# Kernel tuning notes

Hardware: AMD Instinct MI355X
Metric: run time of the kernel (lower is better)

## Reference

```python
import jax, jax.numpy as jnp
import numpy as np

E, D_IN, D_OUT, N = 8, 1024, 1024, 8192

def setup_inputs() -> dict:
    key = jax.random.key(0)
    ks = jax.random.split(key, 5)
    s_in = 1.0 / np.sqrt(D_IN)
    x = jax.random.normal(ks[0], (N, D_IN), dtype=jnp.float32)
    We = jax.random.uniform(ks[1], (E, D_IN, D_OUT), dtype=jnp.float32, minval=-s_in, maxval=s_in)
    be = jax.random.uniform(ks[2], (E, D_OUT), dtype=jnp.float32, minval=-s_in, maxval=s_in)
    Wg = jax.random.uniform(ks[3], (D_IN, E), dtype=jnp.float32, minval=-s_in, maxval=s_in)
    bg = jax.random.uniform(ks[4], (E,), dtype=jnp.float32, minval=-s_in, maxval=s_in)
    return {"x": x, "We": We, "be": be, "Wg": Wg, "bg": bg}

def reference(x, We, be, Wg, bg):
    # experts_outputs: [N, E, D_OUT] (stacked per-expert Linear outputs)
    expert_out = jnp.einsum('ni,eio->neo', x, We) + be[None, :, :]
    # gate: softmax over experts, [N, E]
    gate = jax.nn.softmax(x @ Wg + bg, axis=1)
    # weighted combine (bmm of [N,1,E] x [N,E,D_OUT]) -> [N, D_OUT]
    return jnp.einsum('ne,neo->no', gate, expert_out)
```

## Files before the change

kernel.cpp:

```cpp
#include <hip/hip_runtime.h>
#include <hip/hip_bf16.h>
#include <cstdint>

#define NTOK 8192
#define DIN  1024
#define DOUT 1024
#define NEXP 8

typedef __attribute__((ext_vector_type(8)))  __bf16 bf16x8;
typedef __attribute__((ext_vector_type(4)))  float  f32x4;

__device__ __forceinline__ unsigned short f2bf(float f) {
    unsigned int u = __builtin_bit_cast(unsigned int, f);
    u += 0x7FFFu + ((u >> 16) & 1u);
    return (unsigned short)(u >> 16);
}

__device__ __forceinline__ void cp16(const void* gsrc, void* ldst) {
    __builtin_amdgcn_global_load_lds(
        (const __attribute__((address_space(1))) void*)gsrc,
        (__attribute__((address_space(3))) void*)ldst,
        16, 0, 0);
}

#define BAR() asm volatile("s_barrier" ::: "memory")

__global__ __launch_bounds__(256) void prep_kernel(
    const float* __restrict__ x, const float* __restrict__ We,
    const float* __restrict__ Wg, const float* __restrict__ bg,
    unsigned short* __restrict__ xb, unsigned short* __restrict__ wt,
    float* __restrict__ g)
{
    __shared__ float smem[12416];

    int t = threadIdx.x;

    if (blockIdx.x < 2048) {
        unsigned short* tile = (unsigned short*)smem;
        int b = blockIdx.x;
        int e  = b >> 8;
        int kt = (b >> 4) & 15;
        int ot = b & 15;

        const float* src = We + ((size_t)e << 20) + (size_t)(kt * 64) * DOUT + ot * 64;
        unsigned short* dst = wt + ((size_t)e << 20) + (size_t)(ot * 64) * DIN + kt * 64;

        int kl = t >> 2;
        int og = (t & 3) * 16;
#pragma unroll
        for (int c = 0; c < 4; ++c) {
            int o = og + c * 4;
            float4 v = *(const float4*)&src[(size_t)kl * DOUT + o];
            ushort4 u;
            u.x = f2bf(v.x); u.y = f2bf(v.y); u.z = f2bf(v.z); u.w = f2bf(v.w);
            *(ushort4*)&tile[kl * 72 + o] = u;
        }
        __syncthreads();
        int ol = t >> 2;
        int kg = (t & 3) * 16;
        unsigned short tmp[16];
#pragma unroll
        for (int i = 0; i < 16; ++i) tmp[i] = tile[(kg + i) * 72 + ol];
        *(uint4*)&dst[(size_t)ol * DIN + kg]     = *(uint4*)&tmp[0];
        *(uint4*)&dst[(size_t)ol * DIN + kg + 8] = *(uint4*)&tmp[8];
    } else {
        float* WgL = smem;
        float* xL  = smem + 8192;
        int n0 = (blockIdx.x - 2048) * 32;

#pragma unroll
        for (int q = 0; q < 8; ++q) {
            int fidx = q * 256 + t;
            int k  = fidx >> 1;
            int eh = (fidx & 1) * 4;
            float4 v = *(const float4*)&Wg[(size_t)k * 8 + eh];
            WgL[(eh + 0) * 1024 + k] = v.x;
            WgL[(eh + 1) * 1024 + k] = v.y;
            WgL[(eh + 2) * 1024 + k] = v.z;
            WgL[(eh + 3) * 1024 + k] = v.w;
        }

        int tt = t & 31;
        int e  = t >> 5;
        float acc = 0.f;

        for (int c = 0; c < 8; ++c) {
            int kb = c * 128;
#pragma unroll
            for (int q = 0; q < 4; ++q) {
                int fidx = q * 256 + t;
                int row = fidx >> 5;
                int kk  = (fidx & 31) * 4;
                float4 v = *(const float4*)&x[(size_t)(n0 + row) * DIN + kb + kk];
                ushort4 u;
                u.x = f2bf(v.x); u.y = f2bf(v.y); u.z = f2bf(v.z); u.w = f2bf(v.w);
                *(ushort4*)&xb[(size_t)(n0 + row) * DIN + kb + kk] = u;
                *(float4*)&xL[row * 132 + kk] = v;
            }
            __syncthreads();
#pragma unroll
            for (int kk = 0; kk < 128; kk += 4) {
                float4 xv = *(const float4*)&xL[tt * 132 + kk];
                float4 wv = *(const float4*)&WgL[e * 1024 + kb + kk];
                acc += xv.x * wv.x + xv.y * wv.y + xv.z * wv.z + xv.w * wv.w;
            }
            __syncthreads();
        }

        float* lg = xL;
        lg[tt * 8 + e] = acc + bg[e];
        __syncthreads();
        if (t < 32) {
            float l[8];
#pragma unroll
            for (int i = 0; i < 8; ++i) l[i] = lg[t * 8 + i];
            float m = l[0];
#pragma unroll
            for (int i = 1; i < 8; ++i) m = fmaxf(m, l[i]);
            float s = 0.f;
#pragma unroll
            for (int i = 0; i < 8; ++i) { l[i] = __expf(l[i] - m); s += l[i]; }
            float inv = 1.0f / s;
            float4 p0 = make_float4(l[0]*inv, l[1]*inv, l[2]*inv, l[3]*inv);
            float4 p1 = make_float4(l[4]*inv, l[5]*inv, l[6]*inv, l[7]*inv);
            *(float4*)&g[(size_t)(n0 + tt) * 8]     = p0;
            *(float4*)&g[(size_t)(n0 + tt) * 8 + 4] = p1;
        }
    }
}

__global__ __launch_bounds__(512, 2) void moe_gemm_kernel(
    const unsigned short* __restrict__ xb,
    const unsigned short* __restrict__ wt,
    const float* __restrict__ g,
    const float* __restrict__ be,
    float* __restrict__ out)
{
    __shared__ unsigned short lA[2][256 * 64];
    __shared__ unsigned short lB[2][256 * 64];

    int bid = blockIdx.x;
    int xcd = bid & 7;
    int wl  = bid >> 3;
    int bn  = xcd * 4 + (wl & 3);
    int bm  = wl >> 2;

    int tid  = threadIdx.x;
    int lane = tid & 63;
    int wave = tid >> 6;
    int wm = wave >> 1;
    int wn = wave & 1;

    int rA   = lane & 15;
    int quad = lane >> 4;
    int swz  = rA & 7;

    int srow   = tid >> 3;
    int schunk = ((tid & 7) ^ (srow & 7)) << 3;
    int wOff   = wave * 512;

    const unsigned short* aP0 = xb + (size_t)(bm * 256 + srow) * DIN + schunk;
    const unsigned short* aP1 = aP0 + (size_t)64 * DIN;
    const unsigned short* aP2 = aP0 + (size_t)128 * DIN;
    const unsigned short* aP3 = aP0 + (size_t)192 * DIN;
    int eHi = srow >> 5;
    int col = srow & 31;
    const unsigned short* bP0 = wt + ((size_t)(0 + eHi) << 20) + (size_t)(bn * 32 + col) * DIN + schunk;
    const unsigned short* bP1 = wt + ((size_t)(2 + eHi) << 20) + (size_t)(bn * 32 + col) * DIN + schunk;
    const unsigned short* bP2 = wt + ((size_t)(4 + eHi) << 20) + (size_t)(bn * 32 + col) * DIN + schunk;
    const unsigned short* bP3 = wt + ((size_t)(6 + eHi) << 20) + (size_t)(bn * 32 + col) * DIN + schunk;

    cp16(aP0, &lA[0][0 * 4096 + wOff]);
    cp16(aP1, &lA[0][1 * 4096 + wOff]);
    cp16(aP2, &lA[0][2 * 4096 + wOff]);
    cp16(aP3, &lA[0][3 * 4096 + wOff]);
    cp16(bP0, &lB[0][0 * 4096 + wOff]);
    cp16(bP1, &lB[0][1 * 4096 + wOff]);
    cp16(bP2, &lB[0][2 * 4096 + wOff]);
    cp16(bP3, &lB[0][3 * 4096 + wOff]);

    f32x4 acc[8][4] = {};

    asm volatile("s_waitcnt vmcnt(0)" ::: "memory");
    BAR();

#pragma unroll 1
    for (int t = 0; t < 16; ++t) {
        if (t < 15) {
            int nb = (t + 1) & 1;
            size_t ko = (size_t)(t + 1) * 64;
            cp16(aP0 + ko, &lA[nb][0 * 4096 + wOff]);
            cp16(aP1 + ko, &lA[nb][1 * 4096 + wOff]);
            cp16(aP2 + ko, &lA[nb][2 * 4096 + wOff]);
            cp16(aP3 + ko, &lA[nb][3 * 4096 + wOff]);
            cp16(bP0 + ko, &lB[nb][0 * 4096 + wOff]);
            cp16(bP1 + ko, &lB[nb][1 * 4096 + wOff]);
            cp16(bP2 + ko, &lB[nb][2 * 4096 + wOff]);
            cp16(bP3 + ko, &lB[nb][3 * 4096 + wOff]);
        }

        const unsigned short* A = lA[t & 1];
        const unsigned short* B = lB[t & 1];
#pragma unroll
        for (int h = 0; h < 2; ++h) {
            int kp = ((quad + h * 4) ^ swz) << 3;
            bf16x8 af[4];
#pragma unroll
            for (int i = 0; i < 4; ++i)
                af[i] = *(const bf16x8*)&A[(wm * 64 + i * 16 + rA) * 64 + kp];
            __builtin_amdgcn_s_setprio(1);
#pragma unroll
            for (int e = 0; e < 8; ++e) {
                bf16x8 bfr = *(const bf16x8*)&B[(e * 32 + wn * 16 + rA) * 64 + kp];
#pragma unroll
                for (int i = 0; i < 4; ++i)
                    acc[e][i] = __builtin_amdgcn_mfma_f32_16x16x32_bf16(
                        af[i], bfr, acc[e][i], 0, 0, 0);
            }
            __builtin_amdgcn_s_setprio(0);
        }

        if (t < 15) {
            asm volatile("s_waitcnt vmcnt(0)" ::: "memory");
            BAR();
        }
    }

    int colg = bn * 32 + wn * 16 + rA;
    float bcol[8];
#pragma unroll
    for (int e = 0; e < 8; ++e) bcol[e] = be[(size_t)e * DOUT + colg];
#pragma unroll
    for (int i = 0; i < 4; ++i) {
        int rbase = bm * 256 + wm * 64 + i * 16 + quad * 4;
#pragma unroll
        for (int rr = 0; rr < 4; ++rr) {
            const float* gp = &g[(size_t)(rbase + rr) * 8];
            float4 g0 = *(const float4*)gp;
            float4 g1 = *(const float4*)(gp + 4);
            float s = g0.x * (acc[0][i][rr] + bcol[0])
                    + g0.y * (acc[1][i][rr] + bcol[1])
                    + g0.z * (acc[2][i][rr] + bcol[2])
                    + g0.w * (acc[3][i][rr] + bcol[3])
                    + g1.x * (acc[4][i][rr] + bcol[4])
                    + g1.y * (acc[5][i][rr] + bcol[5])
                    + g1.z * (acc[6][i][rr] + bcol[6])
                    + g1.w * (acc[7][i][rr] + bcol[7]);
            out[(size_t)(rbase + rr) * DOUT + colg] = s;
        }
    }
}

extern "C" void kernel_launch(void* const* d_in, const int* in_sizes, int n_in,
                              void* d_out, int out_size, void* d_ws, size_t ws_size,
                              hipStream_t stream)
{
    const float* x  = (const float*)d_in[0];
    const float* We = (const float*)d_in[1];
    const float* be = (const float*)d_in[2];
    const float* Wg = (const float*)d_in[3];
    const float* bg = (const float*)d_in[4];
    float* out = (float*)d_out;

    unsigned short* xb = (unsigned short*)d_ws;
    unsigned short* wt = xb + (size_t)NTOK * DIN;
    float* g = (float*)(wt + (size_t)NEXP * DOUT * DIN);

    prep_kernel<<<2048 + 256, 256, 0, stream>>>(x, We, Wg, bg, xb, wt, g);
    moe_gemm_kernel<<<(NTOK / 256) * (DOUT / 32), 512, 0, stream>>>(xb, wt, g, be, out);
}
```

Before: 267.1 us.

## Interleave next-tile staging across four compute phases with partial waits

Splits each K-iteration into four phases, each computing two experts. The loads for the next tile are issued in quarters between phases, with barriers in between and a partial vmcnt wait, so global-to-LDS copies are spread across the iteration instead of landing in one burst. All A fragments are loaded up front for both k-halves. The goal is smoother overlap of memory traffic with MFMA work, at the cost of four barriers per iteration instead of one and more live registers.

```diff
diff --git a/kernel.cpp b/kernel.cpp
--- a/kernel.cpp
+++ b/kernel.cpp
@@ -154,76 +154,123 @@
     int rA   = lane & 15;
     int quad = lane >> 4;
     int swz  = rA & 7;
+    int kp0  = (quad       ^ swz) << 3;
+    int kp1  = ((quad + 4) ^ swz) << 3;
 
     int srow   = tid >> 3;
     int schunk = ((tid & 7) ^ (srow & 7)) << 3;
     int wOff   = wave * 512;
 
-    const unsigned short* aP0 = xb + (size_t)(bm * 256 + srow) * DIN + schunk;
-    const unsigned short* aP1 = aP0 + (size_t)64 * DIN;
-    const unsigned short* aP2 = aP0 + (size_t)128 * DIN;
-    const unsigned short* aP3 = aP0 + (size_t)192 * DIN;
-    int eHi = srow >> 5;
-    int col = srow & 31;
-    const unsigned short* bP0 = wt + ((size_t)(0 + eHi) << 20) + (size_t)(bn * 32 + col) * DIN + schunk;
-    const unsigned short* bP1 = wt + ((size_t)(2 + eHi) << 20) + (size_t)(bn * 32 + col) * DIN + schunk;
-    const unsigned short* bP2 = wt + ((size_t)(4 + eHi) << 20) + (size_t)(bn * 32 + col) * DIN + schunk;
-    const unsigned short* bP3 = wt + ((size_t)(6 + eHi) << 20) + (size_t)(bn * 32 + col) * DIN + schunk;
-
-    cp16(aP0, &lA[0][0 * 4096 + wOff]);
-    cp16(aP1, &lA[0][1 * 4096 + wOff]);
-    cp16(aP2, &lA[0][2 * 4096 + wOff]);
-    cp16(aP3, &lA[0][3 * 4096 + wOff]);
-    cp16(bP0, &lB[0][0 * 4096 + wOff]);
-    cp16(bP1, &lB[0][1 * 4096 + wOff]);
-    cp16(bP2, &lB[0][2 * 4096 + wOff]);
-    cp16(bP3, &lB[0][3 * 4096 + wOff]);
+    const unsigned short* aBase = xb + (size_t)(bm * 256 + srow) * DIN + schunk;
+    int eLo  = srow >> 5;
+    int colB = srow & 31;
+    const unsigned short* bBase = wt + (size_t)(bn * 32 + colB) * DIN + schunk;
+
+#define STAGE_A(b, tt, H)                                                        \
+    {   size_t ko = (size_t)(tt) * 64;                                           \
+        cp16(aBase + (size_t)((H) * 128 +  0) * DIN + ko,                        \
+             &lA[b][(H) * 8192 + 0 * 4096 + wOff]);                              \
+        cp16(aBase + (size_t)((H) * 128 + 64) * DIN + ko,                        \
+             &lA[b][(H) * 8192 + 1 * 4096 + wOff]); }
+#define STAGE_B(b, tt, H)                                                        \
+    {   size_t ko = (size_t)(tt) * 64;                                           \
+        cp16(bBase + (((size_t)((H) * 4 + 0 + eLo)) << 20) + ko,                 \
+             &lB[b][(H) * 8192 + 0 * 4096 + wOff]);                              \
+        cp16(bBase + (((size_t)((H) * 4 + 2 + eLo)) << 20) + ko,                 \
+             &lB[b][(H) * 8192 + 1 * 4096 + wOff]); }
+
+    STAGE_A(0, 0, 0); STAGE_A(0, 0, 1);
+    STAGE_B(0, 0, 0); STAGE_B(0, 0, 1);
 
     f32x4 acc[8][4] = {};
-
-    asm volatile("s_waitcnt vmcnt(0)" ::: "memory");
-    BAR();
 
 #pragma unroll 1
     for (int t = 0; t < 16; ++t) {
-        if (t < 15) {
-            int nb = (t + 1) & 1;
-            size_t ko = (size_t)(t + 1) * 64;
-            cp16(aP0 + ko, &lA[nb][0 * 4096 + wOff]);
-            cp16(aP1 + ko, &lA[nb][1 * 4096 + wOff]);
-            cp16(aP2 + ko, &lA[nb][2 * 4096 + wOff]);
-            cp16(aP3 + ko, &lA[nb][3 * 4096 + wOff]);
-            cp16(bP0 + ko, &lB[nb][0 * 4096 + wOff]);
-            cp16(bP1 + ko, &lB[nb][1 * 4096 + wOff]);
-            cp16(bP2 + ko, &lB[nb][2 * 4096 + wOff]);
-            cp16(bP3 + ko, &lB[nb][3 * 4096 + wOff]);
-        }
-
-        const unsigned short* A = lA[t & 1];
-        const unsigned short* B = lB[t & 1];
-#pragma unroll
-        for (int h = 0; h < 2; ++h) {
-            int kp = ((quad + h * 4) ^ swz) << 3;
-            bf16x8 af[4];
-#pragma unroll
-            for (int i = 0; i < 4; ++i)
-                af[i] = *(const bf16x8*)&A[(wm * 64 + i * 16 + rA) * 64 + kp];
+        int c = t & 1, n = c ^ 1;
+        const unsigned short* A = lA[c];
+        const unsigned short* B = lB[c];
+
+        if (t < 15) { STAGE_A(n, t + 1, 0);
+                      asm volatile("s_waitcnt vmcnt(2)" ::: "memory"); }
+        else        { asm volatile("s_waitcnt vmcnt(0)" ::: "memory"); }
+        BAR();
+
+        bf16x8 af[4][2];
+#pragma unroll
+        for (int i = 0; i < 4; ++i) {
+            af[i][0] = *(const bf16x8*)&A[(wm * 64 + i * 16 + rA) * 64 + kp0];
+            af[i][1] = *(const bf16x8*)&A[(wm * 64 + i * 16 + rA) * 64 + kp1];
+        }
+        {
+            bf16x8 b0h0 = *(const bf16x8*)&B[(0 * 32 + wn * 16 + rA) * 64 + kp0];
+            bf16x8 b0h1 = *(const bf16x8*)&B[(0 * 32 + wn * 16 + rA) * 64 + kp1];
+            bf16x8 b1h0 = *(const bf16x8*)&B[(1 * 32 + wn * 16 + rA) * 64 + kp0];
+            bf16x8 b1h1 = *(const bf16x8*)&B[(1 * 32 + wn * 16 + rA) * 64 + kp1];
             __builtin_amdgcn_s_setprio(1);
 #pragma unroll
-            for (int e = 0; e < 8; ++e) {
-                bf16x8 bfr = *(const bf16x8*)&B[(e * 32 + wn * 16 + rA) * 64 + kp];
-#pragma unroll
-                for (int i = 0; i < 4; ++i)
-                    acc[e][i] = __builtin_amdgcn_mfma_f32_16x16x32_bf16(
-                        af[i], bfr, acc[e][i], 0, 0, 0);
+            for (int i = 0; i < 4; ++i) {
+                acc[0][i] = __builtin_amdgcn_mfma_f32_16x16x32_bf16(af[i][0], b0h0, acc[0][i], 0, 0, 0);
+                acc[0][i] = __builtin_amdgcn_mfma_f32_16x16x32_bf16(af[i][1], b0h1, acc[0][i], 0, 0, 0);
+                acc[1][i] = __builtin_amdgcn_mfma_f32_16x16x32_bf16(af[i][0], b1h0, acc[1][i], 0, 0, 0);
+                acc[1][i] = __builtin_amdgcn_mfma_f32_16x16x32_bf16(af[i][1], b1h1, acc[1][i], 0, 0, 0);
             }
             __builtin_amdgcn_s_setprio(0);
         }
-
-        if (t < 15) {
-            asm volatile("s_waitcnt vmcnt(0)" ::: "memory");
-            BAR();
-        }
+        BAR();
+
+        if (t < 15) STAGE_A(n, t + 1, 1);
+        {
+            bf16x8 b0h0 = *(const bf16x8*)&B[(2 * 32 + wn * 16 + rA) * 64 + kp0];
+            bf16x8 b0h1 = *(const bf16x8*)&B[(2 * 32 + wn * 16 + rA) * 64 + kp1];
+            bf16x8 b1h0 = *(const bf16x8*)&B[(3 * 32 + wn * 16 + rA) * 64 + kp0];
+            bf16x8 b1h1 = *(const bf16x8*)&B[(3 * 32 + wn * 16 + rA) * 64 + kp1];
+            __builtin_amdgcn_s_setprio(1);
+#pragma unroll
+            for (int i = 0; i < 4; ++i) {
+                acc[2][i] = __builtin_amdgcn_mfma_f32_16x16x32_bf16(af[i][0], b0h0, acc[2][i], 0, 0, 0);
+                acc[2][i] = __builtin_amdgcn_mfma_f32_16x16x32_bf16(af[i][1], b0h1, acc[2][i], 0, 0, 0);
+                acc[3][i] = __builtin_amdgcn_mfma_f32_16x16x32_bf16(af[i][0], b1h0, acc[3][i], 0, 0, 0);
+                acc[3][i] = __builtin_amdgcn_mfma_f32_16x16x32_bf16(af[i][1], b1h1, acc[3][i], 0, 0, 0);
+            }
+            __builtin_amdgcn_s_setprio(0);
+        }
+        BAR();
+
+        if (t < 15) STAGE_B(n, t + 1, 0);
+        {
+            bf16x8 b0h0 = *(const bf16x8*)&B[(4 * 32 + wn * 16 + rA) * 64 + kp0];
+            bf16x8 b0h1 = *(const bf16x8*)&B[(4 * 32 + wn * 16 + rA) * 64 + kp1];
+            bf16x8 b1h0 = *(const bf16x8*)&B[(5 * 32 + wn * 16 + rA) * 64 + kp0];
+            bf16x8 b1h1 = *(const bf16x8*)&B[(5 * 32 + wn * 16 + rA) * 64 + kp1];
+            __builtin_amdgcn_s_setprio(1);
+#pragma unroll
+            for (int i = 0; i < 4; ++i) {
+                acc[4][i] = __builtin_amdgcn_mfma_f32_16x16x32_bf16(af[i][0], b0h0, acc[4][i], 0, 0, 0);
+                acc[4][i] = __builtin_amdgcn_mfma_f32_16x16x32_bf16(af[i][1], b0h1, acc[4][i], 0, 0, 0);
+                acc[5][i] = __builtin_amdgcn_mfma_f32_16x16x32_bf16(af[i][0], b1h0, acc[5][i], 0, 0, 0);
+                acc[5][i] = __builtin_amdgcn_mfma_f32_16x16x32_bf16(af[i][1], b1h1, acc[5][i], 0, 0, 0);
+            }
+            __builtin_amdgcn_s_setprio(0);
+        }
+        BAR();
+
+        if (t < 15) STAGE_B(n, t + 1, 1);
+        {
+            bf16x8 b0h0 = *(const bf16x8*)&B[(6 * 32 + wn * 16 + rA) * 64 + kp0];
+            bf16x8 b0h1 = *(const bf16x8*)&B[(6 * 32 + wn * 16 + rA) * 64 + kp1];
+            bf16x8 b1h0 = *(const bf16x8*)&B[(7 * 32 + wn * 16 + rA) * 64 + kp0];
+            bf16x8 b1h1 = *(const bf16x8*)&B[(7 * 32 + wn * 16 + rA) * 64 + kp1];
+            __builtin_amdgcn_s_setprio(1);
+#pragma unroll
+            for (int i = 0; i < 4; ++i) {
+                acc[6][i] = __builtin_amdgcn_mfma_f32_16x16x32_bf16(af[i][0], b0h0, acc[6][i], 0, 0, 0);
+                acc[6][i] = __builtin_amdgcn_mfma_f32_16x16x32_bf16(af[i][1], b0h1, acc[6][i], 0, 0, 0);
+                acc[7][i] = __builtin_amdgcn_mfma_f32_16x16x32_bf16(af[i][0], b1h0, acc[7][i], 0, 0, 0);
+                acc[7][i] = __builtin_amdgcn_mfma_f32_16x16x32_bf16(af[i][1], b1h1, acc[7][i], 0, 0, 0);
+            }
+            __builtin_amdgcn_s_setprio(0);
+        }
+        BAR();
     }
 
     int colg = bn * 32 + wn * 16 + rA;
```

Result: faster. 261.8 us (-2.0%).

## Halve GEMM block tile to 128 rows with 256 threads and K-step 32

Applied to the files above, without the earlier changes.

Shrinks each GEMM workgroup from 256 token rows and 8 waves to 128 rows and 4 waves, and halves the K tile from 64 to 32, so the loop runs 32 iterations and uses a new 4-chunk XOR swizzle. The block count doubles and LDS per block drops, which should raise occupancy and give better load balance across CUs. In exchange, each tile of expert weights is reused across fewer token rows, so weight traffic roughly doubles, and there are twice as many barriers per K sweep.

```diff
diff --git a/kernel.cpp b/kernel.cpp
--- a/kernel.cpp
+++ b/kernel.cpp
@@ -129,55 +129,61 @@
     }
 }
 
-__global__ __launch_bounds__(512, 2) void moe_gemm_kernel(
+__global__ __launch_bounds__(256, 2) void moe_gemm_kernel(
     const unsigned short* __restrict__ xb,
     const unsigned short* __restrict__ wt,
     const float* __restrict__ g,
     const float* __restrict__ be,
     float* __restrict__ out)
 {
-    __shared__ unsigned short lA[2][256 * 64];
-    __shared__ unsigned short lB[2][256 * 64];
+    __shared__ unsigned short lA[2][128 * 32];
+    __shared__ unsigned short lB[2][256 * 32];
 
     int bid = blockIdx.x;
     int xcd = bid & 7;
-    int wl  = bid >> 3;
-    int bn  = xcd * 4 + (wl & 3);
-    int bm  = wl >> 2;
+    int idx = bid >> 3;
+    int bn  = xcd * 4 + (idx & 3);
+    int bm  = idx >> 2;
 
     int tid  = threadIdx.x;
     int lane = tid & 63;
     int wave = tid >> 6;
-    int wm = wave >> 1;
-    int wn = wave & 1;
+    int wm   = wave >> 1;
+    int wn   = wave & 1;
 
     int rA   = lane & 15;
     int quad = lane >> 4;
-    int swz  = rA & 7;
-
-    int srow   = tid >> 3;
-    int schunk = ((tid & 7) ^ (srow & 7)) << 3;
-    int wOff   = wave * 512;
-
-    const unsigned short* aP0 = xb + (size_t)(bm * 256 + srow) * DIN + schunk;
-    const unsigned short* aP1 = aP0 + (size_t)64 * DIN;
-    const unsigned short* aP2 = aP0 + (size_t)128 * DIN;
-    const unsigned short* aP3 = aP0 + (size_t)192 * DIN;
-    int eHi = srow >> 5;
-    int col = srow & 31;
-    const unsigned short* bP0 = wt + ((size_t)(0 + eHi) << 20) + (size_t)(bn * 32 + col) * DIN + schunk;
-    const unsigned short* bP1 = wt + ((size_t)(2 + eHi) << 20) + (size_t)(bn * 32 + col) * DIN + schunk;
-    const unsigned short* bP2 = wt + ((size_t)(4 + eHi) << 20) + (size_t)(bn * 32 + col) * DIN + schunk;
-    const unsigned short* bP3 = wt + ((size_t)(6 + eHi) << 20) + (size_t)(bn * 32 + col) * DIN + schunk;
-
-    cp16(aP0, &lA[0][0 * 4096 + wOff]);
-    cp16(aP1, &lA[0][1 * 4096 + wOff]);
-    cp16(aP2, &lA[0][2 * 4096 + wOff]);
-    cp16(aP3, &lA[0][3 * 4096 + wOff]);
-    cp16(bP0, &lB[0][0 * 4096 + wOff]);
-    cp16(bP1, &lB[0][1 * 4096 + wOff]);
-    cp16(bP2, &lB[0][2 * 4096 + wOff]);
-    cp16(bP3, &lB[0][3 * 4096 + wOff]);
+    int kp   = ((quad ^ ((rA >> 1) & 3)) << 3);
+
+    int aRow[4], bRow[8];
+#pragma unroll
+    for (int i = 0; i < 4; ++i) aRow[i] = (wm * 64 + i * 16 + rA) * 32;
+#pragma unroll
+    for (int e = 0; e < 8; ++e) bRow[e] = (e * 32 + wn * 16 + rA) * 32;
+
+    int srow   = tid >> 2;
+    int soff   = ((tid & 3) ^ ((srow >> 1) & 3)) << 3;
+    int sdst   = tid * 8;
+
+    const unsigned short* aS0 = xb + (size_t)(bm * 128 +  0 + srow) * DIN + soff;
+    const unsigned short* aS1 = xb + (size_t)(bm * 128 + 64 + srow) * DIN + soff;
+    int eh   = srow >> 5;
+    int colS = srow & 31;
+    const unsigned short* bS0 = wt + ((size_t)(0 + eh) << 20) + (size_t)(bn * 32 + colS) * DIN + soff;
+    const unsigned short* bS1 = wt + ((size_t)(2 + eh) << 20) + (size_t)(bn * 32 + colS) * DIN + soff;
+    const unsigned short* bS2 = wt + ((size_t)(4 + eh) << 20) + (size_t)(bn * 32 + colS) * DIN + soff;
+    const unsigned short* bS3 = wt + ((size_t)(6 + eh) << 20) + (size_t)(bn * 32 + colS) * DIN + soff;
+
+#define STAGE(b, tt)                                                           \
+    {   size_t ko = (size_t)(tt) * 32;                                         \
+        cp16(aS0 + ko, &lA[b][0 * 2048 + sdst]);                               \
+        cp16(aS1 + ko, &lA[b][1 * 2048 + sdst]);                               \
+        cp16(bS0 + ko, &lB[b][0 * 2048 + sdst]);                               \
+        cp16(bS1 + ko, &lB[b][1 * 2048 + sdst]);                               \
+        cp16(bS2 + ko, &lB[b][2 * 2048 + sdst]);                               \
+        cp16(bS3 + ko, &lB[b][3 * 2048 + sdst]); }
+
+    STAGE(0, 0);
 
     f32x4 acc[8][4] = {};
 
@@ -185,42 +191,28 @@
     BAR();
 
 #pragma unroll 1
-    for (int t = 0; t < 16; ++t) {
-        if (t < 15) {
-            int nb = (t + 1) & 1;
-            size_t ko = (size_t)(t + 1) * 64;
-            cp16(aP0 + ko, &lA[nb][0 * 4096 + wOff]);
-            cp16(aP1 + ko, &lA[nb][1 * 4096 + wOff]);
-            cp16(aP2 + ko, &lA[nb][2 * 4096 + wOff]);
-            cp16(aP3 + ko, &lA[nb][3 * 4096 + wOff]);
-            cp16(bP0 + ko, &lB[nb][0 * 4096 + wOff]);
-            cp16(bP1 + ko, &lB[nb][1 * 4096 + wOff]);
-            cp16(bP2 + ko, &lB[nb][2 * 4096 + wOff]);
-            cp16(bP3 + ko, &lB[nb][3 * 4096 + wOff]);
-        }
-
-        const unsigned short* A = lA[t & 1];
-        const unsigned short* B = lB[t & 1];
-#pragma unroll
-        for (int h = 0; h < 2; ++h) {
-            int kp = ((quad + h * 4) ^ swz) << 3;
-            bf16x8 af[4];
+    for (int t = 0; t < 32; ++t) {
+        int c = t & 1, n = c ^ 1;
+        if (t < 31) STAGE(n, t + 1);
+
+        const unsigned short* A = lA[c];
+        const unsigned short* B = lB[c];
+        bf16x8 af[4], bf[8];
+#pragma unroll
+        for (int i = 0; i < 4; ++i) af[i] = *(const bf16x8*)&A[aRow[i] + kp];
+#pragma unroll
+        for (int e = 0; e < 8; ++e) bf[e] = *(const bf16x8*)&B[bRow[e] + kp];
+
+        __builtin_amdgcn_s_setprio(1);
+#pragma unroll
+        for (int e = 0; e < 8; ++e)
 #pragma unroll
             for (int i = 0; i < 4; ++i)
-                af[i] = *(const bf16x8*)&A[(wm * 64 + i * 16 + rA) * 64 + kp];
-            __builtin_amdgcn_s_setprio(1);
-#pragma unroll
-            for (int e = 0; e < 8; ++e) {
-                bf16x8 bfr = *(const bf16x8*)&B[(e * 32 + wn * 16 + rA) * 64 + kp];
-#pragma unroll
-                for (int i = 0; i < 4; ++i)
-                    acc[e][i] = __builtin_amdgcn_mfma_f32_16x16x32_bf16(
-                        af[i], bfr, acc[e][i], 0, 0, 0);
-            }
-            __builtin_amdgcn_s_setprio(0);
-        }
-
-        if (t < 15) {
+                acc[e][i] = __builtin_amdgcn_mfma_f32_16x16x32_bf16(
+                    af[i], bf[e], acc[e][i], 0, 0, 0);
+        __builtin_amdgcn_s_setprio(0);
+
+        if (t < 31) {
             asm volatile("s_waitcnt vmcnt(0)" ::: "memory");
             BAR();
         }
@@ -232,7 +224,7 @@
     for (int e = 0; e < 8; ++e) bcol[e] = be[(size_t)e * DOUT + colg];
 #pragma unroll
     for (int i = 0; i < 4; ++i) {
-        int rbase = bm * 256 + wm * 64 + i * 16 + quad * 4;
+        int rbase = bm * 128 + wm * 64 + i * 16 + quad * 4;
 #pragma unroll
         for (int rr = 0; rr < 4; ++rr) {
             const float* gp = &g[(size_t)(rbase + rr) * 8];
@@ -267,5 +259,5 @@
     float* g = (float*)(wt + (size_t)NEXP * DOUT * DIN);
 
     prep_kernel<<<2048 + 256, 256, 0, stream>>>(x, We, Wg, bg, xb, wt, g);
-    moe_gemm_kernel<<<(NTOK / 256) * (DOUT / 32), 512, 0, stream>>>(xb, wt, g, be, out);
-}
+    moe_gemm_kernel<<<(NTOK / 128) * (DOUT / 32), 256, 0, stream>>>(xb, wt, g, be, out);
+}
```

Result: no change. 270.0 us (+1.1%).
